# Kernel tuning notes

Measured on AMD Instinct MI355X. Metric: run time of the kernel, lower is better.

## Reference

```python
import jax, jax.numpy as jnp
import numpy as np

N = 50000
E = 800000
D = 64  # d_s


def _mlp2(x, w1, b1, w2, b2):
    # Linear -> SiLU -> Linear
    return jax.nn.silu(x @ w1 + b1) @ w2 + b2


def setup_inputs() -> dict:
    key = jax.random.key(0)
    ks = jax.random.split(key, 20)
    s = jax.random.normal(ks[0], (N, D), jnp.float32)
    v = jax.random.normal(ks[1], (N, 3), jnp.float32)
    edge_index = jax.random.randint(ks[2], (2, E), 0, N, jnp.int32)
    edge_attr = jax.random.normal(ks[3], (E, D), jnp.float32)
    ev = jax.random.normal(ks[4], (E, 3), jnp.float32)
    edge_vec_unit = ev / jnp.linalg.norm(ev, axis=-1, keepdims=True)

    def lin(k, fan_in, fan_out):
        kw, kb = jax.random.split(k)
        lim = 1.0 / np.sqrt(fan_in)
        w = jax.random.uniform(kw, (fan_in, fan_out), jnp.float32, -lim, lim)
        b = jax.random.uniform(kb, (fan_out,), jnp.float32, -lim, lim)
        return w, b

    ng_w1, ng_b1 = lin(ks[5], D + 1, D)
    ng_w2, ng_b2 = lin(ks[6], D, D)
    eg_w1, eg_b1 = lin(ks[7], D + 1, D)
    eg_w2, eg_b2 = lin(ks[8], D, D)
    mg_w1, mg_b1 = lin(ks[9], 3 * D, 2 * D)
    mg_w2, mg_b2 = lin(ks[10], 2 * D, D)
    pe_w, pe_b = lin(ks[11], D, 1)
    up_w, up_b = lin(ks[12], D, D)
    ln_g = jnp.ones((D,), jnp.float32)
    ln_b = jnp.zeros((D,), jnp.float32)
    return dict(s=s, v=v, edge_index=edge_index, edge_attr=edge_attr,
                edge_vec_unit=edge_vec_unit,
                ng_w1=ng_w1, ng_b1=ng_b1, ng_w2=ng_w2, ng_b2=ng_b2,
                eg_w1=eg_w1, eg_b1=eg_b1, eg_w2=eg_w2, eg_b2=eg_b2,
                mg_w1=mg_w1, mg_b1=mg_b1, mg_w2=mg_w2, mg_b2=mg_b2,
                pe_w=pe_w, pe_b=pe_b, up_w=up_w, up_b=up_b,
                ln_g=ln_g, ln_b=ln_b)


def reference(s, v, edge_index, edge_attr, edge_vec_unit,
              ng_w1, ng_b1, ng_w2, ng_b2,
              eg_w1, eg_b1, eg_w2, eg_b2,
              mg_w1, mg_b1, mg_w2, mg_b2,
              pe_w, pe_b, up_w, up_b, ln_g, ln_b):
    row, col = edge_index[0], edge_index[1]
    s_i, s_j = s[row], s[col]            # (E, D)
    v_i, v_j = v[row], v[col]            # (E, 3)

    dot_ij = jnp.sum(v_i * edge_vec_unit, axis=-1, keepdims=True)
    dot_ji = jnp.sum(v_j * -edge_vec_unit, axis=-1, keepdims=True)
    res_ij = 1.0 - dot_ij
    res_ji = 1.0 - dot_ji
    cross_mag = jnp.linalg.norm(jnp.cross(v_i, v_j), axis=-1, keepdims=True)

    node_feat_i = _mlp2(jnp.concatenate([s_i, res_ij], -1), ng_w1, ng_b1, ng_w2, ng_b2)
    node_feat_j = _mlp2(jnp.concatenate([s_j, res_ji], -1), ng_w1, ng_b1, ng_w2, ng_b2)
    edge_feat = _mlp2(jnp.concatenate([edge_attr, cross_mag], -1), eg_w1, eg_b1, eg_w2, eg_b2)

    msg = _mlp2(jnp.concatenate([node_feat_i, node_feat_j, edge_feat], -1),
                mg_w1, mg_b1, mg_w2, mg_b2)   # (E, D)
    coeff = msg @ pe_w + pe_b                 # (E, 1)
    v_msg = edge_vec_unit * coeff             # (E, 3)

    n = s.shape[0]
    s_agg = jax.ops.segment_sum(msg, row, num_segments=n)    # (N, D)
    v_agg = jax.ops.segment_sum(v_msg, row, num_segments=n)  # (N, 3)

    s_new = s + jax.nn.silu(s_agg) @ up_w + up_b
    mu = jnp.mean(s_new, axis=-1, keepdims=True)
    var = jnp.var(s_new, axis=-1, keepdims=True)
    s_out = (s_new - mu) * jax.lax.rsqrt(var + 1e-5) * ln_g + ln_b

    v_new = v + v_agg
    denom = jnp.maximum(jnp.linalg.norm(v_new, axis=-1, keepdims=True), 1e-6)
    v_out = v_new / denom
    return (s_out, v_out)
```

## Files before the change

### kernel.cpp

```cpp
#include <hip/hip_runtime.h>
#include <math.h>

#define NN 50000
#define NE 800000
#define D 64

typedef __attribute__((ext_vector_type(8))) short short8;
typedef __attribute__((ext_vector_type(4))) float f32x4;

__device__ __forceinline__ float silu_f(float x) { return x / (1.0f + __expf(-x)); }

__device__ __forceinline__ unsigned int pack2(float a, float b) {
  unsigned int r;
  asm("v_cvt_pk_bf16_f32 %0, %1, %2" : "=v"(r) : "v"(a), "v"(b));
  return r;
}
__device__ __forceinline__ short8 pack_frag(f32x4 a, f32x4 b) {
  union { unsigned int u[4]; short8 s; } r;
  r.u[0] = pack2(a[0], a[1]);
  r.u[1] = pack2(a[2], a[3]);
  r.u[2] = pack2(b[0], b[1]);
  r.u[3] = pack2(b[2], b[3]);
  return r.s;
}

__global__ void prep_comb(const float* __restrict__ ng_w2,
                          const float* __restrict__ eg_w2,
                          const float* __restrict__ mg_w1,
                          const float* __restrict__ mg_b1,
                          const float* __restrict__ ng_b2,
                          const float* __restrict__ eg_b2,
                          float* __restrict__ W_comb, float* __restrict__ bprime) {
  int t = blockIdx.x * 256 + threadIdx.x;
  if (t < 3 * 64 * 128) {
    int src = t / (64 * 128);
    int r = t % (64 * 128);
    int k = r >> 7, m = r & 127;
    const float* A = (src == 2) ? eg_w2 : ng_w2;
    const float* M = mg_w1 + (size_t)(src * 64) * 128 + m;
    float acc = 0.f;
    for (int n = 0; n < 64; ++n) acc += A[k * 64 + n] * M[(size_t)n * 128];
    W_comb[t] = acc;
  }
  if (t < 128) {
    float acc = mg_b1[t];
    for (int n = 0; n < 64; ++n)
      acc += ng_b2[n] * (mg_w1[(size_t)n * 128 + t] + mg_w1[(size_t)(64 + n) * 128 + t]) +
             eg_b2[n] * mg_w1[(size_t)(128 + n) * 128 + t];
    bprime[t] = acc;
  }
}

__global__ void prep_all(const float* __restrict__ eg_w1,
                         const float* __restrict__ mg_w2,
                         const float* __restrict__ ng_w1,
                         const float* __restrict__ up_w,
                         const float* __restrict__ W_comb,
                         unsigned short* __restrict__ out) {
  int t = blockIdx.x * 256 + threadIdx.x;
  if (t >= 88 * 64) return;
  int frag = t >> 6, L = t & 63;
  const float* W; int N, nt, ks;
  if (frag < 8)       { int lf = frag;      W = eg_w1; N = 64;  nt = lf >> 1; ks = lf & 1; }
  else if (frag < 56) { int lf = frag - 8;  int mt = lf / 6, s2 = lf % 6;
                        W = W_comb + (size_t)(s2 >> 1) * (64 * 128); N = 128;
                        nt = mt; ks = s2 & 1; }
  else if (frag < 72) { int lf = frag - 56; W = mg_w2; N = 64;  nt = lf >> 2; ks = lf & 3; }
  else if (frag < 80) { int lf = frag - 72; W = ng_w1; N = 64;  nt = lf >> 1; ks = lf & 1; }
  else                { int lf = frag - 80; W = up_w;  N = 64;  nt = lf >> 1; ks = lf & 1; }
  int kb = ks * 32 + (L >> 4) * 8;
  int nc = nt * 16 + (L & 15);
  unsigned int p[4];
#pragma unroll
  for (int jj = 0; jj < 4; ++jj) {
    float a = W[(size_t)(kb + 2 * jj) * N + nc];
    float b = W[(size_t)(kb + 2 * jj + 1) * N + nc];
    p[jj] = pack2(a, b);
  }
  *(uint4*)(out + (size_t)frag * 512 + L * 8) = make_uint4(p[0], p[1], p[2], p[3]);
}

__global__ __launch_bounds__(256, 4) void node_pre(
    const float* __restrict__ s, const float* __restrict__ ng_b1,
    const unsigned short* __restrict__ WF, float* __restrict__ h_ng,
    float* __restrict__ s_agg, float* __restrict__ v_agg) {
  __shared__ __align__(16) char sm[4 * 8704];
  int tid = threadIdx.x, w = tid >> 6, lane = tid & 63;
  int l15 = lane & 15, q = lane >> 4, fb = q * 8;
  char* my = sm + w * 8704;
  int nb = (blockIdx.x * 4 + w) * 32;
  if (nb >= NN) return;

  short8 Bs[2][2];
#pragma unroll
  for (int h = 0; h < 2; ++h)
#pragma unroll
    for (int kt = 0; kt < 2; ++kt) {
      int n = nb + h * 16 + l15; if (n >= NN) n = NN - 1;
      f32x4 x0 = *(const f32x4*)(s + (size_t)n * D + kt * 32 + fb);
      f32x4 x1 = *(const f32x4*)(s + (size_t)n * D + kt * 32 + fb + 4);
      Bs[h][kt] = pack_frag(x0, x1);
    }
  short8 F[4][2]; f32x4 bb[4];
#pragma unroll
  for (int mt = 0; mt < 4; ++mt) {
    F[mt][0] = *(const short8*)(WF + (size_t)(72 + mt * 2 + 0) * 512 + lane * 8);
    F[mt][1] = *(const short8*)(WF + (size_t)(72 + mt * 2 + 1) * 512 + lane * 8);
    bb[mt] = *(const f32x4*)(ng_b1 + mt * 16 + 4 * q);
  }
#pragma unroll
  for (int h = 0; h < 2; ++h)
#pragma unroll
    for (int mt = 0; mt < 4; ++mt) {
      f32x4 acc = {0.f, 0.f, 0.f, 0.f};
      acc = __builtin_amdgcn_mfma_f32_16x16x32_bf16(F[mt][0], Bs[h][0], acc, 0, 0, 0);
      acc = __builtin_amdgcn_mfma_f32_16x16x32_bf16(F[mt][1], Bs[h][1], acc, 0, 0, 0);
      acc[0] += bb[mt][0]; acc[1] += bb[mt][1]; acc[2] += bb[mt][2]; acc[3] += bb[mt][3];
      *(f32x4*)(my + (((h * 16 + l15) * 68 + mt * 16 + 4 * q) << 2)) = acc;
    }
#pragma unroll
  for (int h = 0; h < 2; ++h)
#pragma unroll
    for (int e = 0; e < 16; ++e) {
      int n = nb + h * 16 + e;
      if (n < NN) {
        float val = *(const float*)(my + (((h * 16 + e) * 68 + lane) << 2));
        h_ng[(size_t)n * D + lane] = val;
        s_agg[(size_t)n * D + lane] = 0.f;
      }
    }
#pragma unroll
  for (int h = 0; h < 2; ++h) {
    int n = nb + h * 16 + l15;
    if (q < 3 && n < NN) v_agg[(size_t)n * 3 + q] = 0.f;
  }
}

#define LSTR 68
#define LDSW (32 * LSTR * 4)

__global__ __launch_bounds__(256, 4) void edge_mfma(
    const float* __restrict__ v, const int* __restrict__ ei,
    const float* __restrict__ edge_attr, const float* __restrict__ evu,
    const float* __restrict__ ng_w1, const float* __restrict__ eg_w1,
    const float* __restrict__ eg_b1, const float* __restrict__ bprime,
    const float* __restrict__ mg_b2,
    const float* __restrict__ pe_w, const float* __restrict__ pe_b,
    const float* __restrict__ h_ng,
    const unsigned short* __restrict__ WF,
    float* __restrict__ s_agg, float* __restrict__ v_agg) {
  __shared__ __align__(16) char sm[4 * LDSW];
  int tid = threadIdx.x, w = tid >> 6, lane = tid & 63;
  int l15 = lane & 15, q = lane >> 4, fb = q * 8;
  char* my = sm + w * LDSW;
  int eb = (blockIdx.x * 4 + w) * 32;

  int rown[2], coln[2];
  float rij[2], rji[2], uu0[2], uu1[2], uu2[2], cmag[2];
#pragma unroll
  for (int h = 0; h < 2; ++h) {
    int e = eb + h * 16 + l15;
    int r = ei[e], c = ei[NE + e];
    rown[h] = r; coln[h] = c;
    float u0 = evu[e * 3 + 0], u1 = evu[e * 3 + 1], u2 = evu[e * 3 + 2];
    uu0[h] = u0; uu1[h] = u1; uu2[h] = u2;
    float vi0 = v[r * 3 + 0], vi1 = v[r * 3 + 1], vi2 = v[r * 3 + 2];
    float vj0 = v[c * 3 + 0], vj1 = v[c * 3 + 1], vj2 = v[c * 3 + 2];
    rij[h] = 1.f - (vi0 * u0 + vi1 * u1 + vi2 * u2);
    rji[h] = 1.f + (vj0 * u0 + vj1 * u1 + vj2 * u2);
    float cx = vi1 * vj2 - vi2 * vj1;
    float cy = vi2 * vj0 - vi0 * vj2;
    float cz = vi0 * vj1 - vi1 * vj0;
    cmag[h] = sqrtf(cx * cx + cy * cy + cz * cz);
  }

  short8 Bai[2][2], Baj[2][2], Bxe[2][2];
  f32x4 w1l[2][2];
#pragma unroll
  for (int kt = 0; kt < 2; ++kt) {
    w1l[kt][0] = *(const f32x4*)(ng_w1 + 64 * 64 + kt * 32 + fb);
    w1l[kt][1] = *(const f32x4*)(ng_w1 + 64 * 64 + kt * 32 + fb + 4);
  }
#pragma unroll
  for (int h = 0; h < 2; ++h)
#pragma unroll
    for (int kt = 0; kt < 2; ++kt) {
      const float* pr = h_ng + (size_t)rown[h] * D + kt * 32 + fb;
      const float* pc = h_ng + (size_t)coln[h] * D + kt * 32 + fb;
      const float* px = edge_attr + (size_t)(eb + h * 16 + l15) * D + kt * 32 + fb;
      f32x4 a0 = *(const f32x4*)pr, a1 = *(const f32x4*)(pr + 4);
      f32x4 b0 = *(const f32x4*)pc, b1 = *(const f32x4*)(pc + 4);
      f32x4 x0 = *(const f32x4*)px, x1 = *(const f32x4*)(px + 4);
      f32x4 si0, si1, sj0, sj1;
#pragma unroll
      for (int c2 = 0; c2 < 4; ++c2) {
        si0[c2] = silu_f(a0[c2] + rij[h] * w1l[kt][0][c2]);
        si1[c2] = silu_f(a1[c2] + rij[h] * w1l[kt][1][c2]);
        sj0[c2] = silu_f(b0[c2] + rji[h] * w1l[kt][0][c2]);
        sj1[c2] = silu_f(b1[c2] + rji[h] * w1l[kt][1][c2]);
      }
      Bai[h][kt] = pack_frag(si0, si1);
      Baj[h][kt] = pack_frag(sj0, sj1);
      Bxe[h][kt] = pack_frag(x0, x1);
    }

  {
    short8 F[4][2]; f32x4 bb[4], el[4];
#pragma unroll
    for (int mt = 0; mt < 4; ++mt) {
      F[mt][0] = *(const short8*)(WF + (size_t)(0 + mt * 2 + 0) * 512 + lane * 8);
      F[mt][1] = *(const short8*)(WF + (size_t)(0 + mt * 2 + 1) * 512 + lane * 8);
      bb[mt] = *(const f32x4*)(eg_b1 + mt * 16 + 4 * q);
      el[mt] = *(const f32x4*)(eg_w1 + 64 * 64 + mt * 16 + 4 * q);
    }
#pragma unroll
    for (int h = 0; h < 2; ++h)
#pragma unroll
      for (int mt = 0; mt < 4; ++mt) {
        f32x4 acc = {0.f, 0.f, 0.f, 0.f};
        acc = __builtin_amdgcn_mfma_f32_16x16x32_bf16(F[mt][0], Bxe[h][0], acc, 0, 0, 0);
        acc = __builtin_amdgcn_mfma_f32_16x16x32_bf16(F[mt][1], Bxe[h][1], acc, 0, 0, 0);
        float t0 = silu_f(acc[0] + bb[mt][0] + cmag[h] * el[mt][0]);
        float t1 = silu_f(acc[1] + bb[mt][1] + cmag[h] * el[mt][1]);
        float t2 = silu_f(acc[2] + bb[mt][2] + cmag[h] * el[mt][2]);
        float t3 = silu_f(acc[3] + bb[mt][3] + cmag[h] * el[mt][3]);
        uint2 p; p.x = pack2(t0, t1); p.y = pack2(t2, t3);
        *(uint2*)(my + (((h * 16 + l15) * LSTR + mt * 8 + 2 * q) << 2)) = p;
      }
  }

  short8 Bae[2][2];
#pragma unroll
  for (int h = 0; h < 2; ++h)
#pragma unroll
    for (int kt = 0; kt < 2; ++kt)
      Bae[h][kt] = *(const short8*)(my + (((h * 16 + l15) * LSTR + 16 * kt + 4 * q) << 2));

#pragma unroll
  for (int mt = 0; mt < 8; ++mt) {
    short8 F[6];
#pragma unroll
    for (int s2 = 0; s2 < 6; ++s2)
      F[s2] = *(const short8*)(WF + (size_t)(8 + mt * 6 + s2) * 512 + lane * 8);
    f32x4 bb = *(const f32x4*)(bprime + mt * 16 + 4 * q);
#pragma unroll
    for (int h = 0; h < 2; ++h) {
      f32x4 acc = {0.f, 0.f, 0.f, 0.f};
      acc = __builtin_amdgcn_mfma_f32_16x16x32_bf16(F[0], Bai[h][0], acc, 0, 0, 0);
      acc = __builtin_amdgcn_mfma_f32_16x16x32_bf16(F[1], Bai[h][1], acc, 0, 0, 0);
      acc = __builtin_amdgcn_mfma_f32_16x16x32_bf16(F[2], Baj[h][0], acc, 0, 0, 0);
      acc = __builtin_amdgcn_mfma_f32_16x16x32_bf16(F[3], Baj[h][1], acc, 0, 0, 0);
      acc = __builtin_amdgcn_mfma_f32_16x16x32_bf16(F[4], Bae[h][0], acc, 0, 0, 0);
      acc = __builtin_amdgcn_mfma_f32_16x16x32_bf16(F[5], Bae[h][1], acc, 0, 0, 0);
      uint2 p;
      p.x = pack2(silu_f(acc[0] + bb[0]), silu_f(acc[1] + bb[1]));
      p.y = pack2(silu_f(acc[2] + bb[2]), silu_f(acc[3] + bb[3]));
      *(uint2*)(my + (((h * 16 + l15) * LSTR + mt * 8 + 2 * q) << 2)) = p;
    }
  }

  f32x4 msg[2][4];
  {
    short8 Bh[2][4];
#pragma unroll
    for (int h = 0; h < 2; ++h)
#pragma unroll
      for (int kt = 0; kt < 4; ++kt)
        Bh[h][kt] = *(const short8*)(my + (((h * 16 + l15) * LSTR + 16 * kt + 4 * q) << 2));
#pragma unroll
    for (int mt = 0; mt < 4; ++mt) {
      short8 F[4];
#pragma unroll
      for (int ks = 0; ks < 4; ++ks)
        F[ks] = *(const short8*)(WF + (size_t)(56 + mt * 4 + ks) * 512 + lane * 8);
      f32x4 bb = *(const f32x4*)(mg_b2 + mt * 16 + 4 * q);
#pragma unroll
      for (int h = 0; h < 2; ++h) {
        f32x4 acc = {0.f, 0.f, 0.f, 0.f};
#pragma unroll
        for (int ks = 0; ks < 4; ++ks)
          acc = __builtin_amdgcn_mfma_f32_16x16x32_bf16(F[ks], Bh[h][ks], acc, 0, 0, 0);
        acc[0] += bb[0]; acc[1] += bb[1]; acc[2] += bb[2]; acc[3] += bb[3];
        msg[h][mt] = acc;
      }
    }
  }

  float part[2] = {0.f, 0.f};
#pragma unroll
  for (int mt = 0; mt < 4; ++mt) {
    f32x4 pw4 = *(const f32x4*)(pe_w + mt * 16 + 4 * q);
#pragma unroll
    for (int h = 0; h < 2; ++h)
      part[h] += msg[h][mt][0] * pw4[0] + msg[h][mt][1] * pw4[1] +
                 msg[h][mt][2] * pw4[2] + msg[h][mt][3] * pw4[3];
  }
  float peb = pe_b[0];
#pragma unroll
  for (int h = 0; h < 2; ++h) {
    part[h] += __shfl_xor(part[h], 16, 64);
    part[h] += __shfl_xor(part[h], 32, 64);
    if (q < 3) {
      float uc = (q == 0) ? uu0[h] : ((q == 1) ? uu1[h] : uu2[h]);
      atomicAdd(&v_agg[(size_t)rown[h] * 3 + q], uc * (part[h] + peb));
    }
  }

#pragma unroll
  for (int h = 0; h < 2; ++h)
#pragma unroll
    for (int mt = 0; mt < 4; ++mt)
      *(f32x4*)(my + (((h * 16 + l15) * LSTR + mt * 16 + 4 * q) << 2)) = msg[h][mt];
#pragma unroll
  for (int h = 0; h < 2; ++h)
#pragma unroll
    for (int e = 0; e < 16; ++e) {
      int sr = __builtin_amdgcn_readlane(rown[h], e);
      float val = *(const float*)(my + (((h * 16 + e) * LSTR + lane) << 2));
      atomicAdd(&s_agg[(size_t)sr * D + lane], val);
    }
}

__global__ __launch_bounds__(256, 4) void node_out(
    const float* __restrict__ s, const float* __restrict__ v,
    const float* __restrict__ up_b,
    const float* __restrict__ ln_g, const float* __restrict__ ln_b,
    const float* __restrict__ s_agg, const float* __restrict__ v_agg,
    const unsigned short* __restrict__ WF, float* __restrict__ out) {
  __shared__ __align__(16) char sm[4 * 8704];
  int tid = threadIdx.x, w = tid >> 6, lane = tid & 63;
  int l15 = lane & 15, q = lane >> 4, fb = q * 8;
  char* my = sm + w * 8704;
  int nb = (blockIdx.x * 4 + w) * 32;
  if (nb >= NN) return;

  short8 Bg[2][2];
#pragma unroll
  for (int h = 0; h < 2; ++h)
#pragma unroll
    for (int kt = 0; kt < 2; ++kt) {
      int n = nb + h * 16 + l15; if (n >= NN) n = NN - 1;
      f32x4 g0 = *(const f32x4*)(s_agg + (size_t)n * D + kt * 32 + fb);
      f32x4 g1 = *(const f32x4*)(s_agg + (size_t)n * D + kt * 32 + fb + 4);
#pragma unroll
      for (int c2 = 0; c2 < 4; ++c2) { g0[c2] = silu_f(g0[c2]); g1[c2] = silu_f(g1[c2]); }
      Bg[h][kt] = pack_frag(g0, g1);
    }
  short8 F[4][2]; f32x4 bb[4];
#pragma unroll
  for (int mt = 0; mt < 4; ++mt) {
    F[mt][0] = *(const short8*)(WF + (size_t)(80 + mt * 2 + 0) * 512 + lane * 8);
    F[mt][1] = *(const short8*)(WF + (size_t)(80 + mt * 2 + 1) * 512 + lane * 8);
    bb[mt] = *(const f32x4*)(up_b + mt * 16 + 4 * q);
  }
  f32x4 sn[2][4];
#pragma unroll
  for (int h = 0; h < 2; ++h) {
    int n = nb + h * 16 + l15; if (n >= NN) n = NN - 1;
#pragma unroll
    for (int mt = 0; mt < 4; ++mt) {
      f32x4 acc = {0.f, 0.f, 0.f, 0.f};
      acc = __builtin_amdgcn_mfma_f32_16x16x32_bf16(F[mt][0], Bg[h][0], acc, 0, 0, 0);
      acc = __builtin_amdgcn_mfma_f32_16x16x32_bf16(F[mt][1], Bg[h][1], acc, 0, 0, 0);
      f32x4 sv = *(const f32x4*)(s + (size_t)n * D + mt * 16 + 4 * q);
      sn[h][mt][0] = acc[0] + bb[mt][0] + sv[0];
      sn[h][mt][1] = acc[1] + bb[mt][1] + sv[1];
      sn[h][mt][2] = acc[2] + bb[mt][2] + sv[2];
      sn[h][mt][3] = acc[3] + bb[mt][3] + sv[3];
    }
  }
#pragma unroll
  for (int h = 0; h < 2; ++h) {
    float m = 0.f;
#pragma unroll
    for (int mt = 0; mt < 4; ++mt)
      m += sn[h][mt][0] + sn[h][mt][1] + sn[h][mt][2] + sn[h][mt][3];
    m += __shfl_xor(m, 16, 64);
    m += __shfl_xor(m, 32, 64);
    float mu = m * (1.f / 64.f);
    float vv = 0.f;
#pragma unroll
    for (int mt = 0; mt < 4; ++mt)
#pragma unroll
      for (int r = 0; r < 4; ++r) {
        float d = sn[h][mt][r] - mu;
        vv += d * d;
      }
    vv += __shfl_xor(vv, 16, 64);
    vv += __shfl_xor(vv, 32, 64);
    float inv = 1.f / sqrtf(vv * (1.f / 64.f) + 1e-5f);
#pragma unroll
    for (int mt = 0; mt < 4; ++mt) {
      f32x4 lg = *(const f32x4*)(ln_g + mt * 16 + 4 * q);
      f32x4 lb = *(const f32x4*)(ln_b + mt * 16 + 4 * q);
      f32x4 ov;
#pragma unroll
      for (int r = 0; r < 4; ++r) ov[r] = (sn[h][mt][r] - mu) * inv * lg[r] + lb[r];
      *(f32x4*)(my + (((h * 16 + l15) * 68 + mt * 16 + 4 * q) << 2)) = ov;
    }
  }
#pragma unroll
  for (int h = 0; h < 2; ++h)
#pragma unroll
    for (int e = 0; e < 16; ++e) {
      int n = nb + h * 16 + e;
      if (n < NN) {
        float val = *(const float*)(my + (((h * 16 + e) * 68 + lane) << 2));
        out[(size_t)n * D + lane] = val;
      }
    }
#pragma unroll
  for (int h = 0; h < 2; ++h) {
    int n = nb + h * 16 + l15;
    if (q < 3 && n < NN) {
      float v0 = v[n * 3 + 0] + v_agg[(size_t)n * 3 + 0];
      float v1 = v[n * 3 + 1] + v_agg[(size_t)n * 3 + 1];
      float v2 = v[n * 3 + 2] + v_agg[(size_t)n * 3 + 2];
      float nrm = sqrtf(v0 * v0 + v1 * v1 + v2 * v2);
      float denom = fmaxf(nrm, 1e-6f);
      float val = (q == 0) ? v0 : ((q == 1) ? v1 : v2);
      out[(size_t)NN * D + (size_t)n * 3 + q] = val / denom;
    }
  }
}

extern "C" void kernel_launch(void* const* d_in, const int* in_sizes, int n_in,
                              void* d_out, int out_size, void* d_ws, size_t ws_size,
                              hipStream_t stream) {
  const float* s         = (const float*)d_in[0];
  const float* v         = (const float*)d_in[1];
  const int*   ei        = (const int*)d_in[2];
  const float* edge_attr = (const float*)d_in[3];
  const float* evu       = (const float*)d_in[4];
  const float* ng_w1     = (const float*)d_in[5];
  const float* ng_b1     = (const float*)d_in[6];
  const float* ng_w2     = (const float*)d_in[7];
  const float* ng_b2     = (const float*)d_in[8];
  const float* eg_w1     = (const float*)d_in[9];
  const float* eg_b1     = (const float*)d_in[10];
  const float* eg_w2     = (const float*)d_in[11];
  const float* eg_b2     = (const float*)d_in[12];
  const float* mg_w1     = (const float*)d_in[13];
  const float* mg_b1     = (const float*)d_in[14];
  const float* mg_w2     = (const float*)d_in[15];
  const float* mg_b2     = (const float*)d_in[16];
  const float* pe_w      = (const float*)d_in[17];
  const float* pe_b      = (const float*)d_in[18];
  const float* up_w      = (const float*)d_in[19];
  const float* up_b      = (const float*)d_in[20];
  const float* ln_g      = (const float*)d_in[21];
  const float* ln_b      = (const float*)d_in[22];
  (void)in_sizes; (void)n_in; (void)out_size; (void)ws_size;

  float* out = (float*)d_out;
  char* ws = (char*)d_ws;
  size_t o = 0;
  auto carve = [&](size_t bytes) {
    char* p = ws + o;
    o = (o + bytes + 255) & ~(size_t)255;
    return p;
  };
  float* s_agg       = (float*)carve((size_t)NN * D * 4);
  float* v_agg       = (float*)carve((size_t)NN * 3 * 4);
  unsigned short* WF = (unsigned short*)carve((size_t)88 * 512 * 2);
  float* W_comb      = (float*)carve((size_t)3 * 64 * 128 * 4);
  float* bprime      = (float*)carve((size_t)128 * 4);

  float* h_ng = out;

  prep_comb<<<96, 256, 0, stream>>>(ng_w2, eg_w2, mg_w1, mg_b1, ng_b2, eg_b2,
                                    W_comb, bprime);
  prep_all<<<22, 256, 0, stream>>>(eg_w1, mg_w2, ng_w1, up_w, W_comb, WF);

  int node_blocks = (NN + 127) / 128;
  node_pre<<<node_blocks, 256, 0, stream>>>(s, ng_b1, WF, h_ng, s_agg, v_agg);

  edge_mfma<<<NE / 128, 256, 0, stream>>>(
      v, ei, edge_attr, evu,
      ng_w1, eg_w1, eg_b1, bprime, mg_b2,
      pe_w, pe_b, h_ng, WF, s_agg, v_agg);

  node_out<<<node_blocks, 256, 0, stream>>>(
      s, v, up_b, ln_g, ln_b, s_agg, v_agg, WF, out);
}
```

Baseline: 619.4 us.

## Sort edges by destination row and merge consecutive same-row scatter atomics

Adds a counting-sort pipeline (histogram, single-block scan, permutation) that orders edges by row index. The edge kernel then processes edges in that sorted order and accumulates runs of messages sharing the same row in registers before issuing one atomic per run, instead of one atomic per edge per feature. This is meant to cut global atomic traffic to s_agg, at the cost of three extra kernels per call, a memset, and scattered, non-coalesced reads of edge_attr and evu through the permutation.

```diff
diff --git a/kernel.cpp b/kernel.cpp
--- a/kernel.cpp
+++ b/kernel.cpp
@@ -80,6 +80,54 @@
   *(uint4*)(out + (size_t)frag * 512 + L * 8) = make_uint4(p[0], p[1], p[2], p[3]);
 }
 
+__global__ void hist_k(const int* __restrict__ ei, int* __restrict__ cnt) {
+  int e = blockIdx.x * 256 + threadIdx.x;
+  if (e < NE) atomicAdd(&cnt[ei[e]], 1);
+}
+
+#define SCH ((NN + 1023) / 1024)
+__global__ __launch_bounds__(1024) void scan_k(const int* __restrict__ cnt,
+                                               int* __restrict__ row_start,
+                                               int* __restrict__ cursor) {
+  __shared__ int wsum[16];
+  int t = threadIdx.x, lane = t & 63, w = t >> 6;
+  int base = t * SCH;
+  int s = 0;
+  for (int i = 0; i < SCH; ++i) {
+    int b = base + i;
+    if (b < NN) s += cnt[b];
+  }
+  int v = s;
+#pragma unroll
+  for (int off = 1; off < 64; off <<= 1) {
+    int y = __shfl_up(v, off, 64);
+    if (lane >= off) v += y;
+  }
+  if (lane == 63) wsum[w] = v;
+  __syncthreads();
+  int woff = 0;
+  for (int i = 0; i < w; ++i) woff += wsum[i];
+  int run = woff + v - s;
+  for (int i = 0; i < SCH; ++i) {
+    int b = base + i;
+    if (b < NN) {
+      row_start[b] = run;
+      cursor[b] = run;
+      run += cnt[b];
+    }
+  }
+  if (t == 1023) row_start[NN] = run;
+}
+
+__global__ void perm_k(const int* __restrict__ ei, int* __restrict__ cursor,
+                       int* __restrict__ perm) {
+  int e = blockIdx.x * 256 + threadIdx.x;
+  if (e < NE) {
+    int slot = atomicAdd(&cursor[ei[e]], 1);
+    perm[slot] = e;
+  }
+}
+
 __global__ __launch_bounds__(256, 4) void node_pre(
     const float* __restrict__ s, const float* __restrict__ ng_b1,
     const unsigned short* __restrict__ WF, float* __restrict__ h_ng,
@@ -148,18 +196,20 @@
     const float* __restrict__ pe_w, const float* __restrict__ pe_b,
     const float* __restrict__ h_ng,
     const unsigned short* __restrict__ WF,
+    const int* __restrict__ perm,
     float* __restrict__ s_agg, float* __restrict__ v_agg) {
   __shared__ __align__(16) char sm[4 * LDSW];
   int tid = threadIdx.x, w = tid >> 6, lane = tid & 63;
   int l15 = lane & 15, q = lane >> 4, fb = q * 8;
   char* my = sm + w * LDSW;
-  int eb = (blockIdx.x * 4 + w) * 32;
-
-  int rown[2], coln[2];
+  int sb = (blockIdx.x * 4 + w) * 32;
+
+  int pe[2], rown[2], coln[2];
   float rij[2], rji[2], uu0[2], uu1[2], uu2[2], cmag[2];
 #pragma unroll
   for (int h = 0; h < 2; ++h) {
-    int e = eb + h * 16 + l15;
+    int e = perm[sb + h * 16 + l15];
+    pe[h] = e;
     int r = ei[e], c = ei[NE + e];
     rown[h] = r; coln[h] = c;
     float u0 = evu[e * 3 + 0], u1 = evu[e * 3 + 1], u2 = evu[e * 3 + 2];
@@ -187,7 +237,7 @@
     for (int kt = 0; kt < 2; ++kt) {
       const float* pr = h_ng + (size_t)rown[h] * D + kt * 32 + fb;
       const float* pc = h_ng + (size_t)coln[h] * D + kt * 32 + fb;
-      const float* px = edge_attr + (size_t)(eb + h * 16 + l15) * D + kt * 32 + fb;
+      const float* px = edge_attr + (size_t)pe[h] * D + kt * 32 + fb;
       f32x4 a0 = *(const f32x4*)pr, a1 = *(const f32x4*)(pr + 4);
       f32x4 b0 = *(const f32x4*)pc, b1 = *(const f32x4*)(pc + 4);
       f32x4 x0 = *(const f32x4*)px, x1 = *(const f32x4*)(px + 4);
@@ -311,14 +361,23 @@
 #pragma unroll
     for (int mt = 0; mt < 4; ++mt)
       *(f32x4*)(my + (((h * 16 + l15) * LSTR + mt * 16 + 4 * q) << 2)) = msg[h][mt];
-#pragma unroll
-  for (int h = 0; h < 2; ++h)
-#pragma unroll
-    for (int e = 0; e < 16; ++e) {
-      int sr = __builtin_amdgcn_readlane(rown[h], e);
-      float val = *(const float*)(my + (((h * 16 + e) * LSTR + lane) << 2));
-      atomicAdd(&s_agg[(size_t)sr * D + lane], val);
-    }
+
+  {
+    int prev = __builtin_amdgcn_readlane(rown[0], 0);
+    float acc = 0.f;
+#pragma unroll
+    for (int e = 0; e < 32; ++e) {
+      int sr = __builtin_amdgcn_readlane(rown[e >> 4], e & 15);
+      float val = *(const float*)(my + ((e * LSTR + lane) << 2));
+      if (sr != prev) {
+        atomicAdd(&s_agg[(size_t)prev * D + lane], acc);
+        prev = sr;
+        acc = 0.f;
+      }
+      acc += val;
+    }
+    atomicAdd(&s_agg[(size_t)prev * D + lane], acc);
+  }
 }
 
 __global__ __launch_bounds__(256, 4) void node_out(
@@ -465,20 +524,30 @@
   unsigned short* WF = (unsigned short*)carve((size_t)88 * 512 * 2);
   float* W_comb      = (float*)carve((size_t)3 * 64 * 128 * 4);
   float* bprime      = (float*)carve((size_t)128 * 4);
+  int* cnt           = (int*)carve((size_t)NN * 4);
+  int* cursor        = (int*)carve((size_t)NN * 4);
+  int* row_start     = (int*)carve((size_t)(NN + 1) * 4);
+  int* perm          = (int*)carve((size_t)NE * 4);
 
   float* h_ng = out;
+
+  hipMemsetAsync(cnt, 0, (size_t)NN * 4, stream);
 
   prep_comb<<<96, 256, 0, stream>>>(ng_w2, eg_w2, mg_w1, mg_b1, ng_b2, eg_b2,
                                     W_comb, bprime);
   prep_all<<<22, 256, 0, stream>>>(eg_w1, mg_w2, ng_w1, up_w, W_comb, WF);
 
+  hist_k<<<(NE + 255) / 256, 256, 0, stream>>>(ei, cnt);
+  scan_k<<<1, 1024, 0, stream>>>(cnt, row_start, cursor);
+  perm_k<<<(NE + 255) / 256, 256, 0, stream>>>(ei, cursor, perm);
+
   int node_blocks = (NN + 127) / 128;
   node_pre<<<node_blocks, 256, 0, stream>>>(s, ng_b1, WF, h_ng, s_agg, v_agg);
 
   edge_mfma<<<NE / 128, 256, 0, stream>>>(
       v, ei, edge_attr, evu,
       ng_w1, eg_w1, eg_b1, bprime, mg_b2,
-      pe_w, pe_b, h_ng, WF, s_agg, v_agg);
+      pe_w, pe_b, h_ng, WF, perm, s_agg, v_agg);
 
   node_out<<<node_blocks, 256, 0, stream>>>(
       s, v, up_b, ln_g, ln_b, s_agg, v_agg, WF, out);
```

New measurement: 823.5 us. +32.9%, slower.
